# Performance work log

Hardware: AMD Instinct MI355X
Metric: run time of the kernel (lower is better)

Reference implementation:

```python
import jax, jax.numpy as jnp
import numpy as np

D, K, CIN, CD, COUT = 3, 16, 128, 32, 256
C = CIN + CD                  # 160 = C_in + C_delta after concat
DM = -(-COUT // C)            # depth_multiplier = ceil(C_out / C) = 2
N, I = 4, 2048                # batch, points per cloud; M = N*I = 8192


def _bn(x, g, b, eps=1e-5):
    # BatchNorm1d in training mode: biased batch statistics over dim 0
    mu = x.mean(0)
    v = x.var(0)
    return (x - mu) * jax.lax.rsqrt(v + eps) * g + b


def _knn(p, k):
    # knn_graph over ALL M points (wrapper passes no batch vector), loop=True
    d2 = jnp.sum(p * p, axis=1)
    dist = d2[:, None] + d2[None, :] - 2.0 * (p @ p.T)   # [M,M]
    _, idx = jax.lax.top_k(-dist, k)                     # [M,K], self first
    return idx


def _gconv(t, w, b, M):
    # grouped Conv1d(K, K*K, kernel=K, groups=K): t [M,K,K], w [K(cin), K(out/grp), K(tap)]
    return jnp.einsum('mcl,col->mco', t, w).reshape(M, K * K) + b


def _xconv(xf, pf, idx, w1a, b1a, g1a, be1a, w1b, b1b, g1b, be1b,
           w2, b2, g2a, be2a, wc2a, bc2a, g2b, be2b, wc2b, bc2b, g2c, be2c,
           wcd, bcd, wl, bl):
    M = pf.shape[0]
    rel = pf[idx] - pf[:, None, :]                       # [M,K,D] relative neighbor coords
    # mlp1: lift relative coords to C_delta features
    h = rel.reshape(M * K, D)
    h = _bn(jax.nn.elu(h @ w1a + b1a), g1a, be1a)
    h = _bn(jax.nn.elu(h @ w1b + b1b), g1b, be1b)
    x_star = jnp.concatenate([h.reshape(M, K, CD), xf[idx]], axis=-1)  # [M,K,C]
    x_star = x_star.transpose(0, 2, 1)                   # [M,C,K]
    # mlp2: learn KxK X-transformation from the K*D relative coords
    t = _bn(jax.nn.elu(rel.reshape(M, K * D) @ w2 + b2), g2a, be2a).reshape(M, K, K)
    t = _bn(jax.nn.elu(_gconv(t, wc2a, bc2a, M)), g2b, be2b).reshape(M, K, K)
    t = _bn(_gconv(t, wc2b, bc2b, M), g2c, be2c).reshape(M, K, K)
    xt = jnp.einsum('mck,mkj->mcj', x_star, t)           # [M,C,K] batched matmul
    # depthwise Conv1d(C, C*DM, K, groups=C) collapses K, then final Linear
    y = jnp.einsum('mcl,col->mco', xt, wcd).reshape(M, C * DM) + bcd
    return y @ wl + bl                                   # [M,COUT]


def setup_inputs() -> dict:
    key = jax.random.key(0)
    ks = jax.random.split(key, 16)
    r = lambda k, s: jax.random.normal(k, s, jnp.float32) * 0.1
    return dict(
        x=jax.random.normal(ks[0], (N, I, CIN), jnp.float32),
        pos=jax.random.normal(ks[1], (N, I, D), jnp.float32),
        w1a=r(ks[2], (D, CD)), b1a=r(ks[3], (CD,)), g1a=jnp.ones((CD,)), be1a=jnp.zeros((CD,)),
        w1b=r(ks[4], (CD, CD)), b1b=r(ks[5], (CD,)), g1b=jnp.ones((CD,)), be1b=jnp.zeros((CD,)),
        w2=r(ks[6], (D * K, K * K)), b2=r(ks[7], (K * K,)), g2a=jnp.ones((K * K,)), be2a=jnp.zeros((K * K,)),
        wc2a=r(ks[8], (K, K, K)), bc2a=r(ks[9], (K * K,)), g2b=jnp.ones((K * K,)), be2b=jnp.zeros((K * K,)),
        wc2b=r(ks[10], (K, K, K)), bc2b=r(ks[11], (K * K,)), g2c=jnp.ones((K * K,)), be2c=jnp.zeros((K * K,)),
        wcd=r(ks[12], (C, DM, K)), bcd=r(ks[13], (C * DM,)),
        wl=r(ks[14], (C * DM, COUT)), bl=r(ks[15], (COUT,)),
    )


def reference(x, pos, w1a, b1a, g1a, be1a, w1b, b1b, g1b, be1b,
              w2, b2, g2a, be2a, wc2a, bc2a, g2b, be2b, wc2b, bc2b, g2c, be2c,
              wcd, bcd, wl, bl):
    pf = pos.reshape(N * I, D)
    xf = x.reshape(N * I, CIN)
    idx = _knn(pf, K)
    out = _xconv(xf, pf, idx, w1a, b1a, g1a, be1a, w1b, b1b, g1b, be1b,
                 w2, b2, g2a, be2a, wc2a, bc2a, g2b, be2b, wc2b, bc2b, g2c, be2c,
                 wcd, bcd, wl, bl)
    return out.reshape(N, I, COUT)
```

## Files before the change

### kernel.cpp

```cpp
#include <hip/hip_runtime.h>
#include <math.h>

#define M_PTS 8192
#define MK    131072

typedef __fp16 half2v __attribute__((ext_vector_type(2)));
union H2U { half2v h; unsigned u; };

__device__ __forceinline__ float elu(float v){ return v > 0.f ? v : __expf(v)-1.0f; }

__device__ __forceinline__ unsigned pk_min_u16(unsigned a, unsigned b){
  unsigned r; asm("v_pk_min_u16 %0, %1, %2" : "=v"(r) : "v"(a), "v"(b)); return r;
}
__device__ __forceinline__ unsigned pk_max_u16(unsigned a, unsigned b){
  unsigned r; asm("v_pk_max_u16 %0, %1, %2" : "=v"(r) : "v"(a), "v"(b)); return r;
}

__device__ __forceinline__ unsigned distkey(float4 c, float qx, float qy, float qz, float d2q){
  #pragma clang fp contract(off)
  float dot  = __builtin_fmaf(c.z, qz, __builtin_fmaf(c.y, qy, __builtin_fmaf(c.x, qx, 0.0f)));
  float A    = d2q + c.w;
  float B    = 2.0f * dot;
  float dist = A - B;
  unsigned u = __float_as_uint(dist);
  return u ^ ((unsigned)((int)u >> 31) | 0x80000000u);
}

__global__ __launch_bounds__(256) void knn_kernel(const float* __restrict__ pos,
                                                  int* __restrict__ nidx,
                                                  float* __restrict__ st){
  __shared__ float4 cand[1024];
  __shared__ unsigned long long hits[4][2][64];
  int tid  = threadIdx.x;
  int lane = tid & 63;
  int wv   = tid >> 6;
  int q0   = blockIdx.x*8 + wv*2;
  int q1   = q0 + 1;
  if (blockIdx.x == 0){
    for (int i = tid; i < 2048; i += 256) st[i] = 0.f;
  }
  float qx0 = pos[3*q0], qy0 = pos[3*q0+1], qz0 = pos[3*q0+2];
  float qx1 = pos[3*q1], qy1 = pos[3*q1+1], qz1 = pos[3*q1+2];
  float d2q0, d2q1;
  {
    #pragma clang fp contract(off)
    d2q0 = (qx0*qx0 + qy0*qy0) + qz0*qz0;
    d2q1 = (qx1*qx1 + qy1*qy1) + qz1*qz1;
  }

  unsigned ka[8];
  #pragma unroll
  for (int s=0;s<8;s++) ka[s] = 0xFFFFFFFFu;

  for (int base = 0; base < M_PTS; base += 1024){
    for (int t = tid; t < 1024; t += 256){
      #pragma clang fp contract(off)
      int j = base + t;
      float x = pos[3*j], y = pos[3*j+1], z = pos[3*j+2];
      float d2v = (x*x + y*y) + z*z;
      cand[t] = make_float4(x,y,z,d2v);
    }
    __syncthreads();
    #pragma unroll
    for (int k=0; k<16; k++){
      float4 c = cand[lane + k*64];
      float dot0 = c.x*qx0 + c.y*qy0 + c.z*qz0;
      float dot1 = c.x*qx1 + c.y*qy1 + c.z*qz1;
      float d0 = fmaxf((d2q0 + c.w) - 2.0f*dot0, 0.f);
      float d1 = fmaxf((d2q1 + c.w) - 2.0f*dot1, 0.f);
      H2U pu; pu.h = __builtin_amdgcn_cvt_pkrtz(d0, d1);
      unsigned v = pu.u;
      #pragma unroll
      for (int s=0;s<8;s++){
        unsigned mn = pk_min_u16(v, ka[s]);
        unsigned mx = pk_max_u16(v, ka[s]);
        ka[s] = mn; v = mx;
      }
    }
    __syncthreads();
  }

  unsigned thr16[2];
  #pragma unroll
  for (int qq=0; qq<2; qq++){
    unsigned kq[8];
    #pragma unroll
    for (int s=0;s<8;s++) kq[s] = (qq==0) ? (ka[s] & 0xFFFFu) : (ka[s] >> 16);
    unsigned t16 = 0xFFFFu;
    for (int r=0; r<16; r++){
      unsigned mine = kq[0];
      unsigned best = mine;
      #pragma unroll
      for (int off=32; off>0; off>>=1){
        unsigned o = __shfl_xor(best, off, 64);
        best = min(best, o);
      }
      bool adv = (best == mine);
      #pragma unroll
      for (int s=0;s<7;s++) kq[s] = adv ? kq[s+1] : kq[s];
      kq[7] = adv ? 0xFFFFu : kq[7];
      t16 = best;
    }
    thr16[qq] = t16;
  }
  unsigned t0u = min(thr16[0] + 2u, 0x7C00u);
  unsigned t1u = min(thr16[1] + 2u, 0x7C00u);
  float thrF0, thrF1;
  asm("v_cvt_f32_f16 %0, %1" : "=v"(thrF0) : "v"(t0u));
  asm("v_cvt_f32_f16 %0, %1" : "=v"(thrF1) : "v"(t1u));

  int cnt0 = 0, cnt1 = 0;
  for (int base = 0; base < M_PTS; base += 1024){
    for (int t = tid; t < 1024; t += 256){
      #pragma clang fp contract(off)
      int j = base + t;
      float x = pos[3*j], y = pos[3*j+1], z = pos[3*j+2];
      float d2v = (x*x + y*y) + z*z;
      cand[t] = make_float4(x,y,z,d2v);
    }
    __syncthreads();
    #pragma unroll
    for (int k=0; k<16; k++){
      int j = base + lane + k*64;
      float4 c = cand[lane + k*64];
      float dot0 = c.x*qx0 + c.y*qy0 + c.z*qz0;
      float dot1 = c.x*qx1 + c.y*qy1 + c.z*qz1;
      bool h0 = ((d2q0 + c.w) - 2.0f*dot0) <= thrF0;
      bool h1 = ((d2q1 + c.w) - 2.0f*dot1) <= thrF1;
      unsigned long long m0 = __ballot(h0);
      unsigned long long m1 = __ballot(h1);
      if (m0){
        unsigned u = distkey(c, qx0, qy0, qz0, d2q0);
        if (h0){
          int slot = cnt0 + __popcll(m0 & ((1ull<<lane)-1ull));
          if (slot < 64) hits[wv][0][slot] = ((unsigned long long)u << 32) | (unsigned)j;
        }
        cnt0 += (int)__popcll(m0);
      }
      if (m1){
        unsigned u = distkey(c, qx1, qy1, qz1, d2q1);
        if (h1){
          int slot = cnt1 + __popcll(m1 & ((1ull<<lane)-1ull));
          if (slot < 64) hits[wv][1][slot] = ((unsigned long long)u << 32) | (unsigned)j;
        }
        cnt1 += (int)__popcll(m1);
      }
    }
    __syncthreads();
  }

  #pragma unroll
  for (int qq=0; qq<2; qq++){
    int cc = min(qq == 0 ? cnt0 : cnt1, 64);
    int qo = (qq == 0 ? q0 : q1)*16;
    unsigned long long mine = (lane < cc) ? hits[wv][qq][lane] : ~0ull;
    for (int r=0; r<16; r++){
      unsigned long long best = mine;
      #pragma unroll
      for (int off=32; off>0; off>>=1){
        unsigned long long o = __shfl_xor(best, off, 64);
        best = (o < best) ? o : best;
      }
      if (mine == best) mine = ~0ull;
      if (lane == 0) nidx[qo + r] = (int)(unsigned)best;
    }
  }
}

#define COMPUTE_RELF_8()                                              \
  for (int f = tid; f < 8*48; f += 256){                              \
    int p = f/48, kd = f%48, k = kd/3, d = kd%3;                      \
    int j = nidx[(m0+p)*16 + k];                                      \
    relf[p][kd] = pos[3*j+d] - pos[3*(m0+p)+d];                       \
  }                                                                   \
  __syncthreads();

#define COMPUTE_T1_8(acc)                                             \
  _Pragma("unroll")                                                   \
  for (int p=0;p<8;p++) acc[p] = b2[tid];                             \
  for (int kk=0; kk<48; kk++){                                        \
    float w = w2[kk*256 + tid];                                       \
    _Pragma("unroll")                                                 \
    for (int p=0;p<8;p++) acc[p] += relf[p][kk]*w;                    \
  }

__global__ __launch_bounds__(256) void stats_a_kernel(const float* __restrict__ pos,
    const int* __restrict__ nidx,
    const float* __restrict__ w1a, const float* __restrict__ b1a,
    const float* __restrict__ w2,  const float* __restrict__ b2,
    float* __restrict__ tact,
    float* __restrict__ s1, float* __restrict__ s3){
  int tid = threadIdx.x;
  if (blockIdx.x < 512){
    __shared__ float relS[256][3];
    __shared__ float red[8][64];
    int r = blockIdx.x*256 + tid;
    int m = r >> 4;
    int j = nidx[r];
    relS[tid][0] = pos[3*j  ]-pos[3*m  ];
    relS[tid][1] = pos[3*j+1]-pos[3*m+1];
    relS[tid][2] = pos[3*j+2]-pos[3*m+2];
    __syncthreads();
    int c = tid & 31, g = tid >> 5;
    float w0=w1a[c], w1v=w1a[32+c], w2v=w1a[64+c], b=b1a[c];
    float s=0.f, q=0.f;
    for (int rr=g*32; rr<g*32+32; rr++){
      float h = elu(b + relS[rr][0]*w0 + relS[rr][1]*w1v + relS[rr][2]*w2v);
      s += h; q += h*h;
    }
    red[g][c]=s; red[g][32+c]=q;
    __syncthreads();
    if (tid < 64){
      float a=0.f;
      #pragma unroll
      for (int gg=0;gg<8;gg++) a += red[gg][tid];
      atomicAdd(&s1[tid], a);
    }
  } else {
    __shared__ float relf[8][48];
    int m0 = (blockIdx.x-512)*8;
    COMPUTE_RELF_8();
    float acc[8];
    COMPUTE_T1_8(acc);
    float s=0.f, q=0.f;
    #pragma unroll
    for (int p=0;p<8;p++){
      float v = elu(acc[p]);
      s += v; q += v*v;
      tact[(size_t)(m0+p)*256 + tid] = v;
    }
    atomicAdd(&s3[tid], s); atomicAdd(&s3[256+tid], q);
  }
}

__global__ __launch_bounds__(256) void stats_b_kernel(const float* __restrict__ pos,
    const int* __restrict__ nidx,
    const float* __restrict__ w1a, const float* __restrict__ b1a,
    const float* __restrict__ s1,  const float* __restrict__ g1a, const float* __restrict__ be1a,
    const float* __restrict__ w1b, const float* __restrict__ b1b,
    float* __restrict__ tact,
    const float* __restrict__ s3,  const float* __restrict__ g2a, const float* __restrict__ be2a,
    const float* __restrict__ wc2a,const float* __restrict__ bc2a,
    float* __restrict__ s2, float* __restrict__ s4){
  int tid = threadIdx.x;
  const float invMK = 1.f/(float)MK;
  const float invM  = 1.f/8192.f;
  if (blockIdx.x < 2048){
    __shared__ float xnS[64][33];
    __shared__ float red[8][64];
    __shared__ float muA[32], ivA[32];
    if (tid < 32){
      float mu  = s1[tid]*invMK;
      float var = s1[32+tid]*invMK - mu*mu;
      muA[tid] = mu; ivA[tid] = rsqrtf(var+1e-5f)*g1a[tid];
    }
    __syncthreads();
    {
      int rl = tid >> 2;
      int r  = blockIdx.x*64 + rl;
      int m = r >> 4;
      int j = nidx[r];
      float rx = pos[3*j]-pos[3*m], ry = pos[3*j+1]-pos[3*m+1], rz = pos[3*j+2]-pos[3*m+2];
      int c0 = (tid & 3)*8;
      #pragma unroll
      for (int u=0; u<8; u++){
        int cc = c0 + u;
        float h = elu(b1a[cc] + rx*w1a[cc] + ry*w1a[32+cc] + rz*w1a[64+cc]);
        xnS[rl][cc] = (h-muA[cc])*ivA[cc] + be1a[cc];
      }
    }
    __syncthreads();
    int o = tid & 31, g = tid >> 5;
    float wcol[32];
    #pragma unroll
    for (int cc=0;cc<32;cc++) wcol[cc] = w1b[cc*32+o];
    float bo = b1b[o], s=0.f, q=0.f;
    for (int rr=g*8; rr<g*8+8; rr++){
      float a = bo;
      #pragma unroll
      for (int cc=0;cc<32;cc++) a += xnS[rr][cc]*wcol[cc];
      float v = elu(a);
      s += v; q += v*v;
    }
    red[g][o]=s; red[g][32+o]=q;
    __syncthreads();
    if (tid < 64){
      float a=0.f;
      #pragma unroll
      for (int gg=0;gg<8;gg++) a += red[gg][tid];
      atomicAdd(&s2[tid], a);
    }
  } else {
    __shared__ float tn[8][256];
    int m0 = (blockIdx.x-2048)*8;
    float mu3  = s3[tid]*invM;
    float var3 = s3[256+tid]*invM - mu3*mu3;
    float i3   = rsqrtf(var3+1e-5f)*g2a[tid];
    float bb3  = be2a[tid];
    float tv[8];
    #pragma unroll
    for (int p=0;p<8;p++) tv[p] = tact[(size_t)(m0+p)*256 + tid];
    #pragma unroll
    for (int p=0;p<8;p++) tn[p][tid] = (tv[p]-mu3)*i3 + bb3;
    __syncthreads();
    int c = tid >> 4;
    float wreg[16];
    const float4* wv4 = (const float4*)(wc2a + tid*16);
    #pragma unroll
    for (int v=0; v<4; v++){ float4 f = wv4[v]; wreg[4*v]=f.x; wreg[4*v+1]=f.y; wreg[4*v+2]=f.z; wreg[4*v+3]=f.w; }
    float bias = bc2a[tid];
    float s=0.f, q=0.f;
    #pragma unroll
    for (int p=0;p<8;p++){
      float a2 = bias;
      #pragma unroll
      for (int l=0;l<16;l++) a2 += tn[p][c*16+l]*wreg[l];
      float v = elu(a2);
      s += v; q += v*v;
      tv[p] = v;
    }
    #pragma unroll
    for (int p=0;p<8;p++) tact[(size_t)(m0+p)*256 + tid] = tv[p];
    atomicAdd(&s4[tid], s); atomicAdd(&s4[256+tid], q);
  }
}

__global__ __launch_bounds__(256) void t3_stats_kernel(
    float* __restrict__ tact,
    const float* __restrict__ s4, const float* __restrict__ g2b, const float* __restrict__ be2b,
    const float* __restrict__ wc2b, const float* __restrict__ bc2b, float* __restrict__ s5){
  __shared__ float tn2[8][256];
  int m0 = blockIdx.x*8, tid = threadIdx.x;
  const float invM = 1.f/8192.f;
  float mu4  = s4[tid]*invM;
  float var4 = s4[256+tid]*invM - mu4*mu4;
  float i4   = rsqrtf(var4+1e-5f)*g2b[tid];
  float bb4  = be2b[tid];
  float tv[8];
  #pragma unroll
  for (int p=0;p<8;p++) tv[p] = tact[(size_t)(m0+p)*256 + tid];
  #pragma unroll
  for (int p=0;p<8;p++) tn2[p][tid] = (tv[p]-mu4)*i4 + bb4;
  __syncthreads();
  int c = tid >> 4;
  float w2reg[16];
  { const float4* wv4 = (const float4*)(wc2b + tid*16);
    #pragma unroll
    for (int v=0; v<4; v++){ float4 f = wv4[v]; w2reg[4*v]=f.x; w2reg[4*v+1]=f.y; w2reg[4*v+2]=f.z; w2reg[4*v+3]=f.w; } }
  float bias2 = bc2b[tid];
  float s=0.f, q=0.f;
  #pragma unroll
  for (int p=0;p<8;p++){
    float a3 = bias2;
    #pragma unroll
    for (int l=0;l<16;l++) a3 += tn2[p][c*16+l]*w2reg[l];
    s += a3; q += a3*a3;
    tv[p] = a3;
  }
  #pragma unroll
  for (int p=0;p<8;p++) tact[(size_t)(m0+p)*256 + tid] = tv[p];
  atomicAdd(&s5[tid], s); atomicAdd(&s5[256+tid], q);
}

#define PF 4
__global__ __launch_bounds__(256) void final_kernel(
    const float* __restrict__ x, const float* __restrict__ pos, const int* __restrict__ nidx,
    const float* __restrict__ w1a, const float* __restrict__ b1a,
    const float* __restrict__ g1a, const float* __restrict__ be1a,
    const float* __restrict__ w1b, const float* __restrict__ b1b,
    const float* __restrict__ g1b, const float* __restrict__ be1b,
    const float* __restrict__ g2c, const float* __restrict__ be2c,
    const float* __restrict__ wcd, const float* __restrict__ bcd,
    const float* __restrict__ wl,  const float* __restrict__ bl,
    const float* __restrict__ st,
    float* __restrict__ out){
  __shared__ float tA[PF][256];
  __shared__ float xs[PF*32*17];
  __shared__ float yy[PF][320];
  __shared__ int   sidx[PF*16];
  __shared__ float mu1[32], i1g[32], mu2[32], i2g[32];
  int tid = threadIdx.x;
  int m0  = blockIdx.x*PF;
  const float invMK = 1.f/(float)MK;
  const float invM  = 1.f/8192.f;

  if (tid < PF*16) sidx[tid] = nidx[m0*16 + tid];
  if (tid < 32){
    float mu  = st[tid]*invMK;
    float var = st[32+tid]*invMK - mu*mu;
    mu1[tid] = mu; i1g[tid] = rsqrtf(var+1e-5f)*g1a[tid];
    float mu_2  = st[64+tid]*invMK;
    float var_2 = st[96+tid]*invMK - mu_2*mu_2;
    mu2[tid] = mu_2; i2g[tid] = rsqrtf(var_2+1e-5f)*g1b[tid];
  }
  {
    float mu5 = st[1152+tid]*invM, var5 = st[1408+tid]*invM - mu5*mu5;
    float i5 = rsqrtf(var5+1e-5f)*g2c[tid], bb5 = be2c[tid];
    #pragma unroll
    for (int p=0;p<PF;p++){
      float v = out[(size_t)(m0+p)*256 + tid];
      tA[p][tid] = (v-mu5)*i5 + bb5;
    }
  }
  __syncthreads();

  {
    int row = tid >> 2;
    int p = row >> 4, k = row & 15;
    int q8 = (tid & 3)*8;
    int m = m0 + p;
    int j = sidx[p*16 + k];
    float rx = pos[3*j]-pos[3*m], ry = pos[3*j+1]-pos[3*m+1], rz = pos[3*j+2]-pos[3*m+2];
    float xn[32];
    #pragma unroll
    for (int cc=0; cc<32; cc++){
      float h = elu(b1a[cc] + rx*w1a[cc] + ry*w1a[32+cc] + rz*w1a[64+cc]);
      xn[cc] = (h-mu1[cc])*i1g[cc] + be1a[cc];
    }
    #pragma unroll
    for (int oo=0; oo<8; oo++){
      int o = q8 + oo;
      float a = b1b[o];
      #pragma unroll
      for (int cc=0; cc<32; cc++) a += xn[cc]*w1b[cc*32+o];
      float h2v = elu(a);
      xs[(p*32 + o)*17 + k] = (h2v-mu2[o])*i2g[o] + be1b[o];
    }
  }
  __syncthreads();

  for (int pair = tid; pair < PF*160; pair += 256){
    int p = pair / 160, cch = pair % 160;
    float av[16];
    if (cch < 32){
      #pragma unroll
      for (int k16=0;k16<16;k16++) av[k16] = xs[(p*32+cch)*17 + k16];
    } else {
      #pragma unroll
      for (int k16=0;k16<16;k16++) av[k16] = x[(size_t)sidx[p*16+k16]*128 + (cch-32)];
    }
    float xt[16];
    #pragma unroll
    for (int j16=0;j16<16;j16++) xt[j16]=0.f;
    #pragma unroll
    for (int k16=0;k16<16;k16++){
      float a = av[k16];
      #pragma unroll
      for (int j16=0;j16<16;j16++) xt[j16] += a*tA[p][k16*16+j16];
    }
    float y0 = bcd[cch*2], y1 = bcd[cch*2+1];
    #pragma unroll
    for (int l=0;l<16;l++){
      y0 += xt[l]*wcd[cch*32 + l];
      y1 += xt[l]*wcd[cch*32 + 16 + l];
    }
    yy[p][cch*2] = y0; yy[p][cch*2+1] = y1;
  }
  __syncthreads();

  float accO[PF];
  #pragma unroll
  for (int p=0;p<PF;p++) accO[p] = bl[tid];
  for (int q=0;q<320;q++){
    float w = wl[q*256 + tid];
    #pragma unroll
    for (int p=0;p<PF;p++) accO[p] += yy[p][q]*w;
  }
  #pragma unroll
  for (int p=0;p<PF;p++) out[(size_t)(m0+p)*256 + tid] = accO[p];
}

extern "C" void kernel_launch(void* const* d_in, const int* in_sizes, int n_in,
                              void* d_out, int out_size, void* d_ws, size_t ws_size,
                              hipStream_t stream){
  const float* x    = (const float*)d_in[0];
  const float* pos  = (const float*)d_in[1];
  const float* w1a  = (const float*)d_in[2];
  const float* b1a  = (const float*)d_in[3];
  const float* g1a  = (const float*)d_in[4];
  const float* be1a = (const float*)d_in[5];
  const float* w1b  = (const float*)d_in[6];
  const float* b1b  = (const float*)d_in[7];
  const float* g1b  = (const float*)d_in[8];
  const float* be1b = (const float*)d_in[9];
  const float* w2   = (const float*)d_in[10];
  const float* b2   = (const float*)d_in[11];
  const float* g2a  = (const float*)d_in[12];
  const float* be2a = (const float*)d_in[13];
  const float* wc2a = (const float*)d_in[14];
  const float* bc2a = (const float*)d_in[15];
  const float* g2b  = (const float*)d_in[16];
  const float* be2b = (const float*)d_in[17];
  const float* wc2b = (const float*)d_in[18];
  const float* bc2b = (const float*)d_in[19];
  const float* g2c  = (const float*)d_in[20];
  const float* be2c = (const float*)d_in[21];
  const float* wcd  = (const float*)d_in[22];
  const float* bcd  = (const float*)d_in[23];
  const float* wl   = (const float*)d_in[24];
  const float* bl   = (const float*)d_in[25];
  float* out = (float*)d_out;

  char* ws = (char*)d_ws;
  int*   nidx = (int*)(ws + 0);
  float* st   = (float*)(ws + 524288);
  float* s1 = st;
  float* s2 = st + 64;
  float* s3 = st + 128;
  float* s4 = st + 640;
  float* s5 = st + 1152;

  knn_kernel<<<1024,256,0,stream>>>(pos, nidx, st);
  stats_a_kernel<<<1536,256,0,stream>>>(pos, nidx, w1a, b1a, w2, b2, out, s1, s3);
  stats_b_kernel<<<3072,256,0,stream>>>(pos, nidx, w1a, b1a, s1, g1a, be1a, w1b, b1b,
                                        out, s3, g2a, be2a, wc2a, bc2a, s2, s4);
  t3_stats_kernel<<<1024,256,0,stream>>>(out, s4, g2b, be2b, wc2b, bc2b, s5);
  final_kernel<<<2048,256,0,stream>>>(x, pos, nidx,
                                      w1a, b1a, g1a, be1a, w1b, b1b, g1b, be1b,
                                      g2c, be2c, wcd, bcd, wl, bl, st, out);
}
```

Before: 391.2 us.

## Use bf16 MFMA for the final linear layer with pre-packed weights

Adds a final kernel that handles 8 points per block and computes the 320x256 output linear with bf16 MFMA 16x16x32 instructions. The weights are packed into an MFMA-friendly bf16 layout by extra blocks inside stats_a, and the intermediate activations are converted to bf16 in shared memory. The aim is to replace the scalar fp32 FMA loop for the final GEMM. The cost is reduced precision, and the path only runs when the workspace is large enough.

Result: slower. 399.6 us (+2.1%).

```diff
diff --git a/kernel.cpp b/kernel.cpp
--- a/kernel.cpp
+++ b/kernel.cpp
@@ -4,11 +4,18 @@
 #define M_PTS 8192
 #define MK    131072
 
+typedef __attribute__((ext_vector_type(8))) short bf16x8;
+typedef __attribute__((ext_vector_type(4))) float f32x4;
 typedef __fp16 half2v __attribute__((ext_vector_type(2)));
 union H2U { half2v h; unsigned u; };
 
 __device__ __forceinline__ float elu(float v){ return v > 0.f ? v : __expf(v)-1.0f; }
 
+__device__ __forceinline__ unsigned cvt_pk_bf16(float lo, float hi){
+  unsigned r;
+  asm("v_cvt_pk_bf16_f32 %0, %1, %2" : "=v"(r) : "v"(lo), "v"(hi));
+  return r;
+}
 __device__ __forceinline__ unsigned pk_min_u16(unsigned a, unsigned b){
   unsigned r; asm("v_pk_min_u16 %0, %1, %2" : "=v"(r) : "v"(a), "v"(b)); return r;
 }
@@ -188,6 +195,7 @@
     const int* __restrict__ nidx,
     const float* __restrict__ w1a, const float* __restrict__ b1a,
     const float* __restrict__ w2,  const float* __restrict__ b2,
+    const float* __restrict__ wl,  unsigned short* __restrict__ wlbf,
     float* __restrict__ tact,
     float* __restrict__ s1, float* __restrict__ s3){
   int tid = threadIdx.x;
@@ -216,7 +224,7 @@
       for (int gg=0;gg<8;gg++) a += red[gg][tid];
       atomicAdd(&s1[tid], a);
     }
-  } else {
+  } else if (blockIdx.x < 1536){
     __shared__ float relf[8][48];
     int m0 = (blockIdx.x-512)*8;
     COMPUTE_RELF_8();
@@ -230,6 +238,19 @@
       tact[(size_t)(m0+p)*256 + tid] = v;
     }
     atomicAdd(&s3[tid], s); atomicAdd(&s3[256+tid], q);
+  } else {
+    int t = (blockIdx.x - 1536)*256 + tid;
+    int lane = t & 63;
+    int fr   = t >> 6;
+    int k0   = (fr >> 4)*32 + (lane >> 4)*8;
+    int col  = (fr & 15)*16 + (lane & 15);
+    const float* wp = wl + (size_t)k0*256 + col;
+    uint4 v;
+    v.x = cvt_pk_bf16(wp[0],    wp[256]);
+    v.y = cvt_pk_bf16(wp[512],  wp[768]);
+    v.z = cvt_pk_bf16(wp[1024], wp[1280]);
+    v.w = cvt_pk_bf16(wp[1536], wp[1792]);
+    ((uint4*)wlbf)[t] = v;
   }
 }
 
@@ -360,6 +381,139 @@
   #pragma unroll
   for (int p=0;p<8;p++) tact[(size_t)(m0+p)*256 + tid] = tv[p];
   atomicAdd(&s5[tid], s); atomicAdd(&s5[256+tid], q);
+}
+
+#define PF8 8
+__global__ __launch_bounds__(256) void final_mfma_kernel(
+    const float* __restrict__ x, const float* __restrict__ pos, const int* __restrict__ nidx,
+    const float* __restrict__ w1a, const float* __restrict__ b1a,
+    const float* __restrict__ g1a, const float* __restrict__ be1a,
+    const float* __restrict__ w1b, const float* __restrict__ b1b,
+    const float* __restrict__ g1b, const float* __restrict__ be1b,
+    const float* __restrict__ g2c, const float* __restrict__ be2c,
+    const float* __restrict__ wcd, const float* __restrict__ bcd,
+    const unsigned short* __restrict__ wlbf, const float* __restrict__ bl,
+    const float* __restrict__ st,
+    float* __restrict__ out){
+  __shared__ float tA[PF8][256];
+  __shared__ float xs[PF8*32*17];
+  __shared__ unsigned short yh[16][328];
+  __shared__ int   sidx[PF8*16];
+  __shared__ float mu1[32], i1g[32], mu2[32], i2g[32];
+  int tid = threadIdx.x;
+  int m0  = blockIdx.x*PF8;
+  const float invMK = 1.f/(float)MK;
+  const float invM  = 1.f/8192.f;
+
+  if (tid < PF8*16) sidx[tid] = nidx[m0*16 + tid];
+  if (tid < 32){
+    float mu  = st[tid]*invMK;
+    float var = st[32+tid]*invMK - mu*mu;
+    mu1[tid] = mu; i1g[tid] = rsqrtf(var+1e-5f)*g1a[tid];
+    float mu_2  = st[64+tid]*invMK;
+    float var_2 = st[96+tid]*invMK - mu_2*mu_2;
+    mu2[tid] = mu_2; i2g[tid] = rsqrtf(var_2+1e-5f)*g1b[tid];
+  }
+  {
+    unsigned short* yz = &yh[8][0];
+    for (int i = tid; i < 8*328; i += 256) yz[i] = 0;
+  }
+  {
+    float mu5 = st[1152+tid]*invM, var5 = st[1408+tid]*invM - mu5*mu5;
+    float i5 = rsqrtf(var5+1e-5f)*g2c[tid], bb5 = be2c[tid];
+    #pragma unroll
+    for (int p=0;p<PF8;p++){
+      float v = out[(size_t)(m0+p)*256 + tid];
+      tA[p][tid] = (v-mu5)*i5 + bb5;
+    }
+  }
+  __syncthreads();
+
+  for (int half = 0; half < 2; ++half){
+    int row = half*64 + (tid >> 2);
+    int p = row >> 4, k = row & 15;
+    int q8 = (tid & 3)*8;
+    int m = m0 + p;
+    int j = sidx[row];
+    float rx = pos[3*j]-pos[3*m], ry = pos[3*j+1]-pos[3*m+1], rz = pos[3*j+2]-pos[3*m+2];
+    float xn[32];
+    #pragma unroll
+    for (int cc=0; cc<32; cc++){
+      float h = elu(b1a[cc] + rx*w1a[cc] + ry*w1a[32+cc] + rz*w1a[64+cc]);
+      xn[cc] = (h-mu1[cc])*i1g[cc] + be1a[cc];
+    }
+    #pragma unroll
+    for (int oo=0; oo<8; oo++){
+      int o = q8 + oo;
+      float a = b1b[o];
+      #pragma unroll
+      for (int cc=0; cc<32; cc++) a += xn[cc]*w1b[cc*32+o];
+      float h2v = elu(a);
+      xs[(p*32 + o)*17 + k] = (h2v-mu2[o])*i2g[o] + be1b[o];
+    }
+  }
+  __syncthreads();
+
+  for (int pair = tid; pair < PF8*160; pair += 256){
+    int p = pair / 160, cch = pair % 160;
+    float av[16];
+    if (cch < 32){
+      #pragma unroll
+      for (int k16=0;k16<16;k16++) av[k16] = xs[(p*32+cch)*17 + k16];
+    } else {
+      #pragma unroll
+      for (int k16=0;k16<16;k16++) av[k16] = x[(size_t)sidx[p*16+k16]*128 + (cch-32)];
+    }
+    float xt[16];
+    #pragma unroll
+    for (int j16=0;j16<16;j16++) xt[j16]=0.f;
+    #pragma unroll
+    for (int k16=0;k16<16;k16++){
+      float a = av[k16];
+      #pragma unroll
+      for (int j16=0;j16<16;j16++) xt[j16] += a*tA[p][k16*16+j16];
+    }
+    float y0 = bcd[cch*2], y1 = bcd[cch*2+1];
+    #pragma unroll
+    for (int l=0;l<16;l++){
+      y0 += xt[l]*wcd[cch*32 + l];
+      y1 += xt[l]*wcd[cch*32 + 16 + l];
+    }
+    *(unsigned*)&yh[p][cch*2] = cvt_pk_bf16(y0, y1);
+  }
+  __syncthreads();
+
+  {
+    int lane = tid & 63;
+    int wvi  = tid >> 6;
+    int lrow = lane & 15;
+    int lgrp = lane >> 4;
+    const bf16x8* wb = (const bf16x8*)wlbf;
+    f32x4 acc[4];
+    #pragma unroll
+    for (int nt=0; nt<4; ++nt) acc[nt] = (f32x4){0.f,0.f,0.f,0.f};
+    #pragma unroll 1
+    for (int kt = 0; kt < 10; ++kt){
+      bf16x8 ah = *(const bf16x8*)&yh[lrow][kt*32 + lgrp*8];
+      #pragma unroll
+      for (int nt = 0; nt < 4; ++nt){
+        bf16x8 bh = wb[(size_t)((kt*16 + wvi*4 + nt)*64) + lane];
+        acc[nt] = __builtin_amdgcn_mfma_f32_16x16x32_bf16(ah, bh, acc[nt], 0, 0, 0);
+      }
+    }
+    if (lgrp < 2){
+      #pragma unroll
+      for (int nt=0; nt<4; ++nt){
+        int col = wvi*64 + nt*16 + lrow;
+        float bv = bl[col];
+        #pragma unroll
+        for (int r=0;r<4;r++){
+          int orow = lgrp*4 + r;
+          out[(size_t)(m0+orow)*256 + col] = acc[nt][r] + bv;
+        }
+      }
+    }
+  }
 }
 
 #define PF 4
@@ -509,13 +663,22 @@
   float* s3 = st + 128;
   float* s4 = st + 640;
   float* s5 = st + 1152;
+  bool big = ws_size >= (size_t)696320;
+  unsigned short* wlbf = big ? (unsigned short*)(ws + 532480) : (unsigned short*)0;
 
   knn_kernel<<<1024,256,0,stream>>>(pos, nidx, st);
-  stats_a_kernel<<<1536,256,0,stream>>>(pos, nidx, w1a, b1a, w2, b2, out, s1, s3);
+  stats_a_kernel<<<(big ? 1576 : 1536),256,0,stream>>>(pos, nidx, w1a, b1a, w2, b2,
+                                                       wl, wlbf, out, s1, s3);
   stats_b_kernel<<<3072,256,0,stream>>>(pos, nidx, w1a, b1a, s1, g1a, be1a, w1b, b1b,
                                         out, s3, g2a, be2a, wc2a, bc2a, s2, s4);
   t3_stats_kernel<<<1024,256,0,stream>>>(out, s4, g2b, be2b, wc2b, bc2b, s5);
-  final_kernel<<<2048,256,0,stream>>>(x, pos, nidx,
-                                      w1a, b1a, g1a, be1a, w1b, b1b, g1b, be1b,
-                                      g2c, be2c, wcd, bcd, wl, bl, st, out);
-}
+  if (big){
+    final_mfma_kernel<<<1024,256,0,stream>>>(x, pos, nidx,
+                                             w1a, b1a, g1a, be1a, w1b, b1b, g1b, be1b,
+                                             g2c, be2c, wcd, bcd, wlbf, bl, st, out);
+  } else {
+    final_kernel<<<2048,256,0,stream>>>(x, pos, nidx,
+                                        w1a, b1a, g1a, be1a, w1b, b1b, g1b, be1b,
+                                        g2c, be2c, wcd, bcd, wl, bl, st, out);
+  }
+}
```
